# Performance work log

Hardware: AMD Instinct MI355X
Metric: run time of the kernel (lower is better)

Reference implementation:

```python
import jax, jax.numpy as jnp
import numpy as np
import math

U = 1024      # units
H = 16        # num_head
DH = U // H   # units_head
B = 2
Q = 1024      # query length
M = 1024      # memory length
KL = M + Q    # key length
R = KL + 1    # relative positions length (rel-shift needs k_len+1)
EPS = 1e-7    # K.epsilon()


def setup_inputs() -> dict:
    key = jax.random.key(0)
    ks = jax.random.split(key, 11)
    f32 = jnp.float32
    return {
        "inputs": jax.random.normal(ks[0], (B, Q, U), f32),
        "content": jax.random.normal(ks[1], (B, Q, U), f32),
        "memories": jax.random.normal(ks[2], (B, M, U), f32),
        "relatives": jax.random.normal(ks[3], (B, R, U), f32),
        "segment_mat": jax.random.uniform(ks[4], (B, Q, KL, 2), f32),
        "segment_embed": jax.random.normal(ks[5], (2, U), f32) * 0.02,
        "bias_context": jax.random.normal(ks[6], (U,), f32) * 0.02,
        "bias_relative": jax.random.normal(ks[7], (U,), f32) * 0.02,
        "bias_segment": jax.random.normal(ks[8], (U,), f32) * 0.02,
        "permutation": jax.random.uniform(ks[9], (B, Q, KL), f32),
        "kernel": jax.random.normal(ks[10], (U, 5 * U), f32) * 0.02,
    }


def _heads(x):
    # [B, L, U] -> [B, H, L, DH]
    b, l, _ = x.shape
    return x.reshape(b, l, H, DH).transpose(0, 2, 1, 3)


def _rel_shift(x, klen):
    # Transformer-XL relative shift via reshape trick. x: [B, H, Q, R]
    b, h, q, r = x.shape
    x = x.reshape(b, h, r, q)[:, :, 1:, :].reshape(b, h, q, r - 1)
    return x[:, :, :, :klen]


def reference(inputs, content, memories, relatives, segment_mat, segment_embed,
              bias_context, bias_relative, bias_segment, permutation, kernel):
    k_q = kernel[:, :U]
    k_kv = kernel[:, U:3 * U]
    k_r = kernel[:, 3 * U:4 * U]
    k_o = kernel[:, 4 * U:5 * U]

    full = jnp.concatenate([memories, content], axis=1)          # [B, KL, U]
    w_q = inputs @ k_q                                           # [B, Q, U]
    w_kv = full @ k_kv                                           # [B, KL, 2U]
    w_r = relatives @ k_r                                        # [B, R, U]

    w_k = _heads(w_kv[..., :U])                                  # [B, H, KL, DH]
    w_v = _heads(w_kv[..., U:])                                  # [B, H, KL, DH]

    # content term
    q_c = _heads(w_q + bias_context)                             # [B, H, Q, DH]
    a_context = jnp.einsum('bhqd,bhkd->bhqk', q_c, w_k)

    # relative-position term with rel-shift
    q_r = _heads(w_q + bias_relative)
    w_r_h = _heads(w_r)                                          # [B, H, R, DH]
    a_relative = _rel_shift(jnp.einsum('bhqd,bhrd->bhqr', q_r, w_r_h), KL)

    # segment term
    q_s = _heads(w_q + bias_segment)                             # [B, H, Q, DH]
    seg_e = segment_embed.T.reshape(H, DH, 2)                    # [H, DH, 2]
    qs_seg = jnp.einsum('bhqd,hds->bhqs', q_s, seg_e)            # [B, H, Q, 2]
    a_segment = jnp.einsum('bqks,bhqs->bhqk', segment_mat, qs_seg)

    att = (a_context + a_relative + a_segment) / math.sqrt(DH)   # [B, H, Q, KL]
    e = jnp.exp(att - jnp.max(att, axis=-1, keepdims=True))
    e = e * permutation[:, None, :, :]
    att = e / (jnp.sum(e, axis=-1, keepdims=True) + EPS)

    out = jnp.einsum('bhqk,bhkd->bhqd', att, w_v)                # [B, H, Q, DH]
    out = out.transpose(0, 2, 1, 3).reshape(inputs.shape[0], Q, U)
    return out @ k_o                                             # [B, Q, U]
```

## Files before the change

### kernel.cpp

```cpp
#include <hip/hip_runtime.h>

typedef __bf16 bf16;
typedef unsigned short u16;
typedef unsigned int u32;
typedef __attribute__((ext_vector_type(8))) __bf16 bf16x8;
typedef __attribute__((ext_vector_type(4))) __bf16 bf16x4;
typedef __attribute__((ext_vector_type(4))) float f32x4;
typedef __attribute__((ext_vector_type(8))) float f32x8;

#define SWZ(r, s) (((r) << 3) + ((s) ^ ((r) & 7)))
#define GSW(r, s) (((r) << 2) + ((s) ^ (((r) >> 1) & 3)))

__device__ __forceinline__ f32x4 mfma16(bf16x8 a, bf16x8 b, f32x4 c) {
  return __builtin_amdgcn_mfma_f32_16x16x32_bf16(a, b, c, 0, 0, 0);
}
__device__ __forceinline__ void gld16(const void* g, void* l) {
  __builtin_amdgcn_global_load_lds((const __attribute__((address_space(1))) void*)g,
                                   (__attribute__((address_space(3))) void*)l, 16, 0, 0);
}

__global__ __launch_bounds__(256) void prep_all(
    const float* __restrict__ inputs, const float* __restrict__ mem,
    const float* __restrict__ cont, const float* __restrict__ rel,
    const float* __restrict__ K, bf16* __restrict__ in_b,
    bf16* __restrict__ full_b, bf16* __restrict__ rel_b, bf16* __restrict__ KT) {
  __shared__ float t[64][68];
  const int bid = blockIdx.x, tid = threadIdx.x;
  if (bid < 1024) {
    size_t i = ((size_t)bid * 256 + tid) * 8;
    f32x8 v = *reinterpret_cast<const f32x8*>(inputs + i);
    *reinterpret_cast<bf16x8*>(in_b + i) = __builtin_convertvector(v, bf16x8);
  } else if (bid < 3072) {
    size_t i = ((size_t)(bid - 1024) * 256 + tid) * 8;
    int row = (int)(i >> 10), col = (int)(i & 1023);
    int b = row >> 11, r = row & 2047;
    const float* src = (r < 1024)
        ? (mem  + (((size_t)(b << 10) + r)          << 10) + col)
        : (cont + (((size_t)(b << 10) + (r - 1024)) << 10) + col);
    f32x8 v = *reinterpret_cast<const f32x8*>(src);
    *reinterpret_cast<bf16x8*>(full_b + i) = __builtin_convertvector(v, bf16x8);
  } else if (bid < 5121) {
    size_t i = ((size_t)(bid - 3072) * 256 + tid) * 8;
    f32x8 v = *reinterpret_cast<const f32x8*>(rel + i);
    *reinterpret_cast<bf16x8*>(rel_b + i) = __builtin_convertvector(v, bf16x8);
  } else {
    const int r = bid - 5121;
    const int n0 = (r % 80) << 6, k0 = (r / 80) << 6;
    for (int idx = tid; idx < 1024; idx += 256) {
      int rr = idx >> 4, c4 = (idx & 15) << 2;
      f32x4 v = *reinterpret_cast<const f32x4*>(K + (size_t)(k0 + rr) * 5120 + n0 + c4);
      t[rr][c4] = v.x; t[rr][c4 + 1] = v.y; t[rr][c4 + 2] = v.z; t[rr][c4 + 3] = v.w;
    }
    __syncthreads();
    for (int idx = tid; idx < 1024; idx += 256) {
      int rr = idx >> 4, c4 = (idx & 15) << 2;
      bf16x4 o = { (bf16)t[c4][rr], (bf16)t[c4 + 1][rr], (bf16)t[c4 + 2][rr], (bf16)t[c4 + 3][rr] };
      *reinterpret_cast<bf16x4*>(KT + (size_t)(n0 + rr) * 1024 + k0 + c4) = o;
    }
  }
}

template<int MT, int OUT_MODE, int KLEN, bool KWRAP>
__device__ __forceinline__ void gemm_body(
    const bf16* __restrict__ A, const bf16* __restrict__ BT,
    void* __restrict__ C0v, void* __restrict__ C1v,
    int m0, int n0, int Mrows, int splitN, bf16* As, bf16* Bs, int tid) {
  const int l = tid & 63, w = tid >> 6;
  const int wn = (w & 1) << 6;
  const int wm = (w >> 1) * (MT / 2);
  constexpr int MFR = MT / 32;
  const int lc = l & 15, l16 = l >> 4;
  f32x4 acc[MFR][4] = {};
  const int r0 = tid >> 2;
  const int sq = tid & 3;
  const int g0 = (sq ^ ((r0 >> 1) & 3)) << 3;

  for (int k0 = 0; k0 < KLEN; k0 += 32) {
    const int kk = KWRAP ? (k0 & 1023) : k0;
    __syncthreads();
    gld16(A  + (size_t)(m0 + r0) * KLEN + k0 + g0, &As[tid << 3]);
    gld16(BT + (size_t)(n0 + r0) * 1024 + kk + g0, &Bs[tid << 3]);
    if (MT == 128)
      gld16(A + (size_t)(m0 + r0 + 64) * KLEN + k0 + g0, &As[(tid + 256) << 3]);
    gld16(BT + (size_t)(n0 + r0 + 64) * 1024 + kk + g0, &Bs[(tid + 256) << 3]);
    __syncthreads();
    bf16x8 af[MFR], bfv[4];
#pragma unroll
    for (int m = 0; m < MFR; ++m)
      af[m] = *reinterpret_cast<const bf16x8*>(&As[GSW(wm + (m << 4) + lc, l16) << 3]);
#pragma unroll
    for (int n = 0; n < 4; ++n)
      bfv[n] = *reinterpret_cast<const bf16x8*>(&Bs[GSW(wn + (n << 4) + lc, l16) << 3]);
#pragma unroll
    for (int m = 0; m < MFR; ++m)
#pragma unroll
      for (int n = 0; n < 4; ++n)
        acc[m][n] = mfma16(af[m], bfv[n], acc[m][n]);
  }
#pragma unroll
  for (int m = 0; m < MFR; ++m) {
    const int rbase = m0 + wm + (m << 4) + (l16 << 2);
#pragma unroll
    for (int n = 0; n < 4; ++n) {
      const int col = n0 + wn + (n << 4) + lc;
      const int cc = (col < splitN) ? col : (col - splitN);
      void* Cv = (col < splitN) ? C0v : C1v;
#pragma unroll
      for (int r = 0; r < 4; ++r) {
        const int row = rbase + r;
        if (row < Mrows) {
          const float v = acc[m][n][r];
          const size_t off = ((size_t)row << 10) + cc;
          if (OUT_MODE == 1) ((bf16*)Cv)[off] = (bf16)v;
          else               ((float*)Cv)[off] = v;
        }
      }
    }
  }
}

__global__ __launch_bounds__(256) void proj_fused(
    const bf16* __restrict__ in_b, const bf16* __restrict__ full_b,
    const bf16* __restrict__ rel_b, const bf16* __restrict__ kT,
    bf16* __restrict__ w_q, bf16* __restrict__ w_k, bf16* __restrict__ w_v,
    bf16* __restrict__ w_rh) {
  __shared__ bf16 As[4096];
  __shared__ bf16 Bs[4096];
  const int bid = blockIdx.x, tid = threadIdx.x;
  if (bid < 256) {
    gemm_body<64, 1, 1024, false>(in_b, kT, w_q, w_q,
                                  (bid >> 3) << 6, (bid & 7) << 7, 2048, 1 << 30, As, Bs, tid);
  } else if (bid < 768) {
    const int r = bid - 256;
    gemm_body<128, 1, 1024, false>(full_b, kT + (1 << 20), w_k, w_v,
                                   (r >> 4) << 7, (r & 15) << 7, 4096, 1024, As, Bs, tid);
  } else {
    const int r = bid - 768;
    gemm_body<64, 1, 1024, false>(rel_b, kT + 3 * (1 << 20), w_rh, w_rh,
                                  (r >> 3) << 6, (r & 7) << 7, 4098, 1 << 30, As, Bs, tid);
  }
}

__global__ __launch_bounds__(256) void out_proj(
    const bf16* __restrict__ a_cat, const bf16* __restrict__ kTo,
    float* __restrict__ out) {
  __shared__ bf16 As[4096];
  __shared__ bf16 Bs[4096];
  const int bid = blockIdx.x, tid = threadIdx.x;
  gemm_body<64, 0, 2048, true>(a_cat, kTo, out, out,
                               (bid >> 3) << 6, (bid & 7) << 7, 2048, 1 << 30, As, Bs, tid);
}

__global__ __launch_bounds__(256) void mid_prep(
    const float* __restrict__ seg_mat, bf16* __restrict__ seg_b,
    const bf16* __restrict__ w_q, const float* __restrict__ bias_s,
    const float* __restrict__ seg_embed, float* __restrict__ qs) {
  const int bid = blockIdx.x, tid = threadIdx.x;
  if (bid < 4096) {
    size_t i = ((size_t)bid * 256 + tid) * 8;
    f32x8 v = *reinterpret_cast<const f32x8*>(seg_mat + i);
    *reinterpret_cast<bf16x8*>(seg_b + i) = __builtin_convertvector(v, bf16x8);
  } else {
    int idx = (bid - 4096) * 256 + tid;
    int q = idx & 1023, h = (idx >> 10) & 15, b = idx >> 14;
    const bf16* wp = w_q + (((size_t)(b << 10) + q) << 10) + (h << 6);
    const float* bp = bias_s + (h << 6);
    const float* e0 = seg_embed + (h << 6);
    const float* e1 = seg_embed + 1024 + (h << 6);
    float s0 = 0.f, s1 = 0.f;
#pragma unroll 8
    for (int d = 0; d < 64; ++d) {
      float v = (float)wp[d] + bp[d];
      s0 = fmaf(v, e0[d], s0);
      s1 = fmaf(v, e1[d], s1);
    }
    qs[((size_t)idx << 1) + 0] = s0;
    qs[((size_t)idx << 1) + 1] = s1;
  }
}

__global__ __launch_bounds__(256) void attn_mfma(
    const bf16* __restrict__ w_q, const bf16* __restrict__ w_k,
    const bf16* __restrict__ w_v, const bf16* __restrict__ w_rh,
    const float* __restrict__ qs_seg, const bf16* __restrict__ seg_b,
    const float* __restrict__ perm, const float* __restrict__ bias_c,
    const float* __restrict__ bias_r, bf16* __restrict__ a_cat) {
  const int id = blockIdx.x;
  const int h  = (id >> 3) & 15;
  const int cg = (id & 7) | ((id >> 7) << 3);
  const int qt = cg & 15, b = cg >> 4;
  const int qi0 = qt << 6;
  const int tid = threadIdx.x;
  const int w = tid >> 6, l = tid & 63;
  const int lc = l & 15, l16 = l >> 4;
  const int w16 = w << 4;
  const int myq = w16 + lc;

  __shared__ bf16 kt[2][2048];
  __shared__ u16  vt[2][2560];
  __shared__ bf16 wbc[8192];
  __shared__ bf16 wb2v[4096];
  __shared__ float artf[3840];
  float* artw = &artf[w * 960];
  u16*   plw  = (u16*)artw;

  auto stageK = [&](int buf, int kj) {
    int r = tid >> 3, s = tid & 7;
    gld16(w_k + ((size_t)((b << 11) + kj + r) << 10) + (h << 6) + ((s ^ (r & 7)) << 3),
          &kt[buf][tid << 3]);
  };
  auto stageWB = [&](int L0, int nrows, int OFF) {
    for (int base = 0; base < nrows; base += 32) {
      int r = (tid >> 3) + base, s = tid & 7;
      int L = L0 + r;
      int slot = (L + OFF) & 127;
      int grow = L > 2048 ? 2048 : L;
      gld16(w_rh + ((size_t)(b * 2049 + grow) << 10) + (h << 6) + ((s ^ (slot & 7)) << 3),
            &wbc[((slot << 3) | s) << 3]);
    }
  };
  auto stageWB2 = [&]() {
    for (int base = 0; base < 64; base += 32) {
      int r = (tid >> 3) + base, s = tid & 7;
      gld16(w_rh + ((size_t)(b * 2049 + r) << 10) + (h << 6) + ((s ^ (r & 7)) << 3),
            &wb2v[((r << 3) | s) << 3]);
    }
  };
  const int kv2 = (tid & 15) << 1, d4 = ((tid >> 4) & 15) << 2, kw = tid & 15;
  auto loadV = [&](int kj, uint2& ra, uint2& rb) {
    const u16* vp = (const u16*)w_v + ((size_t)((b << 11) + kj + kv2) << 10) + (h << 6) + d4;
    ra = *reinterpret_cast<const uint2*>(vp);
    rb = *reinterpret_cast<const uint2*>(vp + 1024);
  };
  auto writeV = [&](int buf, uint2 ra, uint2 rb) {
    u32* vt32 = reinterpret_cast<u32*>(&vt[buf][0]);
    vt32[(d4 + 0) * 20 + kw] = (ra.x & 0xffffu) | (rb.x << 16);
    vt32[(d4 + 1) * 20 + kw] = (ra.x >> 16) | (rb.x & 0xffff0000u);
    vt32[(d4 + 2) * 20 + kw] = (ra.y & 0xffffu) | (rb.y << 16);
    vt32[(d4 + 3) * 20 + kw] = (ra.y >> 16) | (rb.y & 0xffff0000u);
  };
  const size_t qrowg = (size_t)((b << 10) + qi0 + myq);
  auto loadSP = [&](int kj, bf16x8& sA, bf16x8& sB, f32x4& pA, f32x4& pB) {
    const bf16* sp = seg_b + (qrowg * 2048 + kj + (l16 << 2)) * 2;
    sA = *reinterpret_cast<const bf16x8*>(sp);
    sB = *reinterpret_cast<const bf16x8*>(sp + 32);
    const float* pp = perm + qrowg * 2048 + kj + (l16 << 2);
    pA = *reinterpret_cast<const f32x4*>(pp);
    pB = *reinterpret_cast<const f32x4*>(pp + 16);
  };
  auto artWr = [&](int bandcol, f32x4 a_) {
    *reinterpret_cast<f32x4*>(&artw[bandcol * 20 + (l16 << 2)]) = a_;
  };
  auto artRd = [&](int col) -> float {
    return artw[col * 20 + lc];
  };

  stageK(0, 0);
  stageWB(961 - qi0, 96, 7);
  uint2 ra0, rb0;
  loadV(0, ra0, rb0);
  bf16x8 segA_c, segB_c, segA_n = {}, segB_n = {};
  f32x4 pmA_c, pmB_c, pmA_n = {}, pmB_n = {};
  loadSP(0, segA_c, segB_c, pmA_c, pmB_c);

  const float SCLF = 0.125f * 1.44269504f;
  const int dlo = l16 << 3;
  bf16x8 qcf0, qcf1, qrf0, qrf1, qrg0, qrg1;
  {
    const bf16* qb  = w_q + ((qrowg) << 10) + (h << 6);
    const int rq1 = (qi0 + myq + 1 > 1023) ? 1023 : qi0 + myq + 1;
    const bf16* qb1 = w_q + (((size_t)(b << 10) + rq1) << 10) + (h << 6);
    f32x8 bc0 = *reinterpret_cast<const f32x8*>(bias_c + (h << 6) + dlo);
    f32x8 bc1 = *reinterpret_cast<const f32x8*>(bias_c + (h << 6) + 32 + dlo);
    f32x8 br0 = *reinterpret_cast<const f32x8*>(bias_r + (h << 6) + dlo);
    f32x8 br1 = *reinterpret_cast<const f32x8*>(bias_r + (h << 6) + 32 + dlo);
    bf16x8 q0 = *reinterpret_cast<const bf16x8*>(qb + dlo);
    bf16x8 q1 = *reinterpret_cast<const bf16x8*>(qb + 32 + dlo);
    bf16x8 p0 = *reinterpret_cast<const bf16x8*>(qb1 + dlo);
    bf16x8 p1 = *reinterpret_cast<const bf16x8*>(qb1 + 32 + dlo);
    qcf0 = __builtin_convertvector((__builtin_convertvector(q0, f32x8) + bc0) * SCLF, bf16x8);
    qcf1 = __builtin_convertvector((__builtin_convertvector(q1, f32x8) + bc1) * SCLF, bf16x8);
    qrf0 = __builtin_convertvector((__builtin_convertvector(q0, f32x8) + br0) * SCLF, bf16x8);
    qrf1 = __builtin_convertvector((__builtin_convertvector(q1, f32x8) + br1) * SCLF, bf16x8);
    qrg0 = __builtin_convertvector((__builtin_convertvector(p0, f32x8) + br0) * SCLF, bf16x8);
    qrg1 = __builtin_convertvector((__builtin_convertvector(p1, f32x8) + br1) * SCLF, bf16x8);
  }
  const float* qp = qs_seg + ((((size_t)((b << 4) + h) << 10) + qi0 + myq) << 1);
  const float qs0 = qp[0] * SCLF, qs1 = qp[1] * SCLF;

  writeV(0, ra0, rb0);
  __syncthreads();

  float mrow = -1e30f, lrow = 0.f;
  f32x4 o[4] = {};
  int cur = 0;
  uint2 ra_n = {}, rb_n = {};

  for (int t = 0; t < 64; ++t) {
    const int kj = t << 5;
    const int rel0 = kj - qi0;
    const bool strad = (rel0 == 1024) | (rel0 == 1056);
    const bool mainB = (rel0 >= 1088);
    const bool spec1088 = (rel0 == 1088);
    const int nxt = cur ^ 1;

    if (t < 63) {
      const int kjn = kj + 32, rel0n = rel0 + 32;
      stageK(nxt, kjn);
      if (rel0n == 1024) stageWB2();
      if (rel0n <= 1056)       stageWB(rel0n + 1025, 32, 7);
      else if (rel0n == 1088)  stageWB(64, 32, 8);
      else if (rel0n == 1120) { stageWB(32, 32, 8); stageWB(96, 32, 8); }
      else                     stageWB(rel0n - 1024, 32, 8);
      loadV(kjn, ra_n, rb_n);
      loadSP(kjn, segA_n, segB_n, pmA_n, pmB_n);
    }

    f32x4 s0 = {0.f, 0.f, 0.f, 0.f}, s1 = {0.f, 0.f, 0.f, 0.f};
    {
      const bf16* ktc = kt[cur];
      bf16x8 a0 = *reinterpret_cast<const bf16x8*>(&ktc[SWZ(lc, l16) << 3]);
      bf16x8 a1 = *reinterpret_cast<const bf16x8*>(&ktc[SWZ(lc, l16 + 4) << 3]);
      bf16x8 a2 = *reinterpret_cast<const bf16x8*>(&ktc[SWZ(16 + lc, l16) << 3]);
      bf16x8 a3 = *reinterpret_cast<const bf16x8*>(&ktc[SWZ(16 + lc, l16 + 4) << 3]);
      s0 = mfma16(a0, qcf0, s0); s0 = mfma16(a1, qcf1, s0);
      s1 = mfma16(a2, qcf0, s1); s1 = mfma16(a3, qcf1, s1);
    }

    float relv[8];
    {
      const bf16x8 ar0 = mainB ? qrg0 : qrf0;
      const bf16x8 ar1 = mainB ? qrg1 : qrf1;
      int sbase;
      if (!mainB) sbase = (rel0 + 1016 - w16) & 127;
      else        sbase = (rel0 - 1032 - w16) & 127;
#pragma unroll
      for (int bg = 0; bg < 3; ++bg) {
        bf16x8 w0, w1;
        if (spec1088) {
          int Lr = 48 - w16 + (bg << 4) + lc;
          const bf16* p0 = (Lr < 64) ? &wb2v[SWZ(Lr, l16) << 3]
                                     : &wbc[SWZ((Lr + 8) & 127, l16) << 3];
          const bf16* p1 = (Lr < 64) ? &wb2v[SWZ(Lr, l16 + 4) << 3]
                                     : &wbc[SWZ((Lr + 8) & 127, l16 + 4) << 3];
          w0 = *reinterpret_cast<const bf16x8*>(p0);
          w1 = *reinterpret_cast<const bf16x8*>(p1);
        } else {
          int prow = (sbase + (bg << 4) + lc) & 127;
          w0 = *reinterpret_cast<const bf16x8*>(&wbc[SWZ(prow, l16) << 3]);
          w1 = *reinterpret_cast<const bf16x8*>(&wbc[SWZ(prow, l16 + 4) << 3]);
        }
        f32x4 a_ = {0.f, 0.f, 0.f, 0.f};
        a_ = mfma16(ar0, w0, a_); a_ = mfma16(ar1, w1, a_);
        artWr((bg << 4) + lc, a_);
      }
#pragma unroll
      for (int jj = 0; jj < 4; ++jj) {
        relv[jj]     = artRd(15 + (l16 << 2) + jj - lc);
        relv[4 + jj] = artRd(31 + (l16 << 2) + jj - lc);
      }
      if (strad) {
#pragma unroll
        for (int bg = 0; bg < 3; ++bg) {
          int srow = rel0 - 1040 - w16 + (bg << 4) + lc;
          srow = srow < 0 ? 0 : (srow > 63 ? 63 : srow);
          bf16x8 w0 = *reinterpret_cast<const bf16x8*>(&wb2v[SWZ(srow, l16) << 3]);
          bf16x8 w1 = *reinterpret_cast<const bf16x8*>(&wb2v[SWZ(srow, l16 + 4) << 3]);
          f32x4 a_ = {0.f, 0.f, 0.f, 0.f};
          a_ = mfma16(qrg0, w0, a_); a_ = mfma16(qrg1, w1, a_);
          artWr((bg << 4) + lc, a_);
        }
#pragma unroll
        for (int jj = 0; jj < 4; ++jj) {
          const int jA = (l16 << 2) + jj, jB = 16 + jA;
          float rbA = artRd(15 + jA - lc);
          float rbB = artRd(15 + jB - lc);
          if (rel0 + jA - myq >= 1025) relv[jj] = rbA;
          if (rel0 + jB - myq >= 1025) relv[4 + jj] = rbB;
        }
      }
    }

    bool full;
    float facr;
    {
      f32x8 sgA = __builtin_convertvector(segA_c, f32x8);
      f32x8 sgB = __builtin_convertvector(segB_c, f32x8);
      float sv[8];
#pragma unroll
      for (int jj = 0; jj < 4; ++jj) {
        sv[jj]     = s0[jj] + relv[jj]     + sgA[2 * jj] * qs0 + sgA[2 * jj + 1] * qs1;
        sv[4 + jj] = s1[jj] + relv[4 + jj] + sgB[2 * jj] * qs0 + sgB[2 * jj + 1] * qs1;
      }
      float tm = sv[0];
#pragma unroll
      for (int jj = 1; jj < 8; ++jj) tm = fmaxf(tm, sv[jj]);
      tm = fmaxf(tm, __shfl_xor(tm, 16));
      tm = fmaxf(tm, __shfl_xor(tm, 32));
      full = __any(tm > mrow + 8.f);
      if (full) {
        const float mn2 = fmaxf(mrow, tm);
        facr = exp2f(mrow - mn2);
        mrow = mn2;
      } else {
        facr = 1.f;
      }
      float e[8], rs = 0.f;
#pragma unroll
      for (int jj = 0; jj < 4; ++jj) {
        e[jj]     = exp2f(sv[jj] - mrow) * pmA_c[jj];
        e[4 + jj] = exp2f(sv[4 + jj] - mrow) * pmB_c[jj];
        rs += e[jj] + e[4 + jj];
      }
      rs += __shfl_xor(rs, 16);
      rs += __shfl_xor(rs, 32);
      lrow = lrow * facr + rs;
      bf16x4 pa, pb;
#pragma unroll
      for (int jj = 0; jj < 4; ++jj) { pa[jj] = (bf16)e[jj]; pb[jj] = (bf16)e[4 + jj]; }
      *reinterpret_cast<bf16x4*>(&plw[lc * 40 + (l16 << 2)]) = pa;
      *reinterpret_cast<bf16x4*>(&plw[lc * 40 + 16 + (l16 << 2)]) = pb;
    }

    {
      if (full) {
        const int r4 = l16 << 2;
        float fr0 = __shfl(facr, r4 + 0);
        float fr1 = __shfl(facr, r4 + 1);
        float fr2 = __shfl(facr, r4 + 2);
        float fr3 = __shfl(facr, r4 + 3);
#pragma unroll
        for (int n = 0; n < 4; ++n) {
          o[n][0] *= fr0; o[n][1] *= fr1; o[n][2] *= fr2; o[n][3] *= fr3;
        }
      }
      bf16x8 ap = *reinterpret_cast<const bf16x8*>(&plw[lc * 40 + (l16 << 3)]);
      bf16x8 bv0 = *reinterpret_cast<const bf16x8*>(&vt[cur][(lc) * 40 + (l16 << 3)]);
      bf16x8 bv1 = *reinterpret_cast<const bf16x8*>(&vt[cur][(16 + lc) * 40 + (l16 << 3)]);
      bf16x8 bv2 = *reinterpret_cast<const bf16x8*>(&vt[cur][(32 + lc) * 40 + (l16 << 3)]);
      bf16x8 bv3 = *reinterpret_cast<const bf16x8*>(&vt[cur][(48 + lc) * 40 + (l16 << 3)]);
      o[0] = mfma16(ap, bv0, o[0]);
      o[1] = mfma16(ap, bv1, o[1]);
      o[2] = mfma16(ap, bv2, o[2]);
      o[3] = mfma16(ap, bv3, o[3]);
    }

    if (t < 63) {
      writeV(nxt, ra_n, rb_n);
      segA_c = segA_n; segB_c = segB_n; pmA_c = pmA_n; pmB_c = pmB_n;
    }
    __syncthreads();
    cur = nxt;
  }

  {
    float inv[4];
#pragma unroll
    for (int r = 0; r < 4; ++r)
      inv[r] = 1.f / (__shfl(lrow, (l16 << 2) + r) + 1e-7f);
#pragma unroll
    for (int n = 0; n < 4; ++n) {
#pragma unroll
      for (int r = 0; r < 4; ++r) {
        const int row = qi0 + w16 + (l16 << 2) + r;
        const float v = o[n][r] * inv[r];
        const bf16 hi = (bf16)v;
        const float lof = v - (float)hi;
        const size_t off = (((size_t)(b << 10) + row) << 11) + (h << 6) + (n << 4) + lc;
        a_cat[off] = hi;
        a_cat[off + 1024] = (bf16)lof;
      }
    }
  }
}

extern "C" void kernel_launch(void* const* d_in, const int* in_sizes, int n_in,
                              void* d_out, int out_size, void* d_ws, size_t ws_size,
                              hipStream_t stream) {
  (void)in_sizes; (void)n_in; (void)out_size; (void)ws_size;
  const float* inputs    = (const float*)d_in[0];
  const float* content   = (const float*)d_in[1];
  const float* memories  = (const float*)d_in[2];
  const float* relatives = (const float*)d_in[3];
  const float* seg_mat   = (const float*)d_in[4];
  const float* seg_embed = (const float*)d_in[5];
  const float* bias_c    = (const float*)d_in[6];
  const float* bias_r    = (const float*)d_in[7];
  const float* bias_s    = (const float*)d_in[8];
  const float* perm      = (const float*)d_in[9];
  const float* kern      = (const float*)d_in[10];
  float* out = (float*)d_out;

  char* ws = (char*)d_ws;
  bf16*  in_b   = (bf16*)(ws);
  bf16*  full_b = (bf16*)(ws + 4194304);
  bf16*  rel_b  = (bf16*)(ws + 12582912);
  bf16*  kT     = (bf16*)(ws + 21233664);
  bf16*  w_q    = (bf16*)(ws + 31719424);
  bf16*  w_k    = (bf16*)(ws + 35913728);
  bf16*  w_v    = (bf16*)(ws + 44302336);
  bf16*  w_rh   = (bf16*)(ws + 52690944);
  float* qs     = (float*)(ws + 65277952);
  bf16*  seg_b  = (bf16*)(ws);
  bf16*  a_cat  = (bf16*)(ws + 21233664);
  bf16*  kTo    = (bf16*)(ws + 29622272);

  dim3 blk(256);
  prep_all<<<6401, blk, 0, stream>>>(inputs, memories, content, relatives, kern,
                                     in_b, full_b, rel_b, kT);
  proj_fused<<<1288, blk, 0, stream>>>(in_b, full_b, rel_b, kT, w_q, w_k, w_v, w_rh);
  mid_prep<<<4224, blk, 0, stream>>>(seg_mat, seg_b, w_q, bias_s, seg_embed, qs);
  attn_mfma<<<512, blk, 0, stream>>>(w_q, w_k, w_v, w_rh, qs, seg_b, perm,
                                     bias_c, bias_r, a_cat);
  out_proj<<<256, blk, 0, stream>>>(a_cat, kTo, out);
}
```

Measured before the change: 260.6 us.

## Fuse segment-matrix conversion and segment query projection into attention kernel

```diff
diff --git a/kernel.cpp b/kernel.cpp
--- a/kernel.cpp
+++ b/kernel.cpp
@@ -151,40 +151,13 @@
                                (bid >> 3) << 6, (bid & 7) << 7, 2048, 1 << 30, As, Bs, tid);
 }
 
-__global__ __launch_bounds__(256) void mid_prep(
-    const float* __restrict__ seg_mat, bf16* __restrict__ seg_b,
-    const bf16* __restrict__ w_q, const float* __restrict__ bias_s,
-    const float* __restrict__ seg_embed, float* __restrict__ qs) {
-  const int bid = blockIdx.x, tid = threadIdx.x;
-  if (bid < 4096) {
-    size_t i = ((size_t)bid * 256 + tid) * 8;
-    f32x8 v = *reinterpret_cast<const f32x8*>(seg_mat + i);
-    *reinterpret_cast<bf16x8*>(seg_b + i) = __builtin_convertvector(v, bf16x8);
-  } else {
-    int idx = (bid - 4096) * 256 + tid;
-    int q = idx & 1023, h = (idx >> 10) & 15, b = idx >> 14;
-    const bf16* wp = w_q + (((size_t)(b << 10) + q) << 10) + (h << 6);
-    const float* bp = bias_s + (h << 6);
-    const float* e0 = seg_embed + (h << 6);
-    const float* e1 = seg_embed + 1024 + (h << 6);
-    float s0 = 0.f, s1 = 0.f;
-#pragma unroll 8
-    for (int d = 0; d < 64; ++d) {
-      float v = (float)wp[d] + bp[d];
-      s0 = fmaf(v, e0[d], s0);
-      s1 = fmaf(v, e1[d], s1);
-    }
-    qs[((size_t)idx << 1) + 0] = s0;
-    qs[((size_t)idx << 1) + 1] = s1;
-  }
-}
-
 __global__ __launch_bounds__(256) void attn_mfma(
     const bf16* __restrict__ w_q, const bf16* __restrict__ w_k,
     const bf16* __restrict__ w_v, const bf16* __restrict__ w_rh,
-    const float* __restrict__ qs_seg, const bf16* __restrict__ seg_b,
-    const float* __restrict__ perm, const float* __restrict__ bias_c,
-    const float* __restrict__ bias_r, bf16* __restrict__ a_cat) {
+    const float* __restrict__ seg_mat, const float* __restrict__ perm,
+    const float* __restrict__ bias_c, const float* __restrict__ bias_r,
+    const float* __restrict__ bias_s, const float* __restrict__ seg_embed,
+    bf16* __restrict__ a_cat) {
   const int id = blockIdx.x;
   const int h  = (id >> 3) & 15;
   const int cg = (id & 7) | ((id >> 7) << 3);
@@ -201,6 +174,7 @@
   __shared__ bf16 wbc[8192];
   __shared__ bf16 wb2v[4096];
   __shared__ float artf[3840];
+  __shared__ float facw[64], lroww[64];
   float* artw = &artf[w * 960];
   u16*   plw  = (u16*)artw;
 
@@ -240,10 +214,10 @@
     vt32[(d4 + 3) * 20 + kw] = (ra.y >> 16) | (rb.y & 0xffff0000u);
   };
   const size_t qrowg = (size_t)((b << 10) + qi0 + myq);
-  auto loadSP = [&](int kj, bf16x8& sA, bf16x8& sB, f32x4& pA, f32x4& pB) {
-    const bf16* sp = seg_b + (qrowg * 2048 + kj + (l16 << 2)) * 2;
-    sA = *reinterpret_cast<const bf16x8*>(sp);
-    sB = *reinterpret_cast<const bf16x8*>(sp + 32);
+  auto loadSP = [&](int kj, f32x8& sA, f32x8& sB, f32x4& pA, f32x4& pB) {
+    const float* sp = seg_mat + (qrowg * 2048 + kj + (l16 << 2)) * 2;
+    sA = *reinterpret_cast<const f32x8*>(sp);
+    sB = *reinterpret_cast<const f32x8*>(sp + 32);
     const float* pp = perm + qrowg * 2048 + kj + (l16 << 2);
     pA = *reinterpret_cast<const f32x4*>(pp);
     pB = *reinterpret_cast<const f32x4*>(pp + 16);
@@ -259,13 +233,14 @@
   stageWB(961 - qi0, 96, 7);
   uint2 ra0, rb0;
   loadV(0, ra0, rb0);
-  bf16x8 segA_c, segB_c, segA_n = {}, segB_n = {};
+  f32x8 segA_c, segB_c, segA_n = {}, segB_n = {};
   f32x4 pmA_c, pmB_c, pmA_n = {}, pmB_n = {};
   loadSP(0, segA_c, segB_c, pmA_c, pmB_c);
 
   const float SCLF = 0.125f * 1.44269504f;
   const int dlo = l16 << 3;
   bf16x8 qcf0, qcf1, qrf0, qrf1, qrg0, qrg1;
+  float qs0, qs1;
   {
     const bf16* qb  = w_q + ((qrowg) << 10) + (h << 6);
     const int rq1 = (qi0 + myq + 1 > 1023) ? 1023 : qi0 + myq + 1;
@@ -278,15 +253,31 @@
     bf16x8 q1 = *reinterpret_cast<const bf16x8*>(qb + 32 + dlo);
     bf16x8 p0 = *reinterpret_cast<const bf16x8*>(qb1 + dlo);
     bf16x8 p1 = *reinterpret_cast<const bf16x8*>(qb1 + 32 + dlo);
-    qcf0 = __builtin_convertvector((__builtin_convertvector(q0, f32x8) + bc0) * SCLF, bf16x8);
-    qcf1 = __builtin_convertvector((__builtin_convertvector(q1, f32x8) + bc1) * SCLF, bf16x8);
-    qrf0 = __builtin_convertvector((__builtin_convertvector(q0, f32x8) + br0) * SCLF, bf16x8);
-    qrf1 = __builtin_convertvector((__builtin_convertvector(q1, f32x8) + br1) * SCLF, bf16x8);
+    f32x8 qf0 = __builtin_convertvector(q0, f32x8);
+    f32x8 qf1 = __builtin_convertvector(q1, f32x8);
+    qcf0 = __builtin_convertvector((qf0 + bc0) * SCLF, bf16x8);
+    qcf1 = __builtin_convertvector((qf1 + bc1) * SCLF, bf16x8);
+    qrf0 = __builtin_convertvector((qf0 + br0) * SCLF, bf16x8);
+    qrf1 = __builtin_convertvector((qf1 + br1) * SCLF, bf16x8);
     qrg0 = __builtin_convertvector((__builtin_convertvector(p0, f32x8) + br0) * SCLF, bf16x8);
     qrg1 = __builtin_convertvector((__builtin_convertvector(p1, f32x8) + br1) * SCLF, bf16x8);
-  }
-  const float* qp = qs_seg + ((((size_t)((b << 4) + h) << 10) + qi0 + myq) << 1);
-  const float qs0 = qp[0] * SCLF, qs1 = qp[1] * SCLF;
+    f32x8 bs0 = *reinterpret_cast<const f32x8*>(bias_s + (h << 6) + dlo);
+    f32x8 bs1 = *reinterpret_cast<const f32x8*>(bias_s + (h << 6) + 32 + dlo);
+    f32x8 e00 = *reinterpret_cast<const f32x8*>(seg_embed + (h << 6) + dlo);
+    f32x8 e01 = *reinterpret_cast<const f32x8*>(seg_embed + (h << 6) + 32 + dlo);
+    f32x8 e10 = *reinterpret_cast<const f32x8*>(seg_embed + 1024 + (h << 6) + dlo);
+    f32x8 e11 = *reinterpret_cast<const f32x8*>(seg_embed + 1024 + (h << 6) + 32 + dlo);
+    f32x8 qa = qf0 + bs0, qb2 = qf1 + bs1;
+    float t0 = 0.f, t1 = 0.f;
+#pragma unroll
+    for (int j = 0; j < 8; ++j) {
+      t0 = fmaf(qa[j], e00[j], fmaf(qb2[j], e01[j], t0));
+      t1 = fmaf(qa[j], e10[j], fmaf(qb2[j], e11[j], t1));
+    }
+    t0 += __shfl_xor(t0, 16); t0 += __shfl_xor(t0, 32);
+    t1 += __shfl_xor(t1, 16); t1 += __shfl_xor(t1, 32);
+    qs0 = t0 * SCLF; qs1 = t1 * SCLF;
+  }
 
   writeV(0, ra0, rb0);
   __syncthreads();
@@ -381,35 +372,26 @@
       }
     }
 
-    bool full;
-    float facr;
     {
-      f32x8 sgA = __builtin_convertvector(segA_c, f32x8);
-      f32x8 sgB = __builtin_convertvector(segB_c, f32x8);
       float sv[8];
 #pragma unroll
       for (int jj = 0; jj < 4; ++jj) {
-        sv[jj]     = s0[jj] + relv[jj]     + sgA[2 * jj] * qs0 + sgA[2 * jj + 1] * qs1;
-        sv[4 + jj] = s1[jj] + relv[4 + jj] + sgB[2 * jj] * qs0 + sgB[2 * jj + 1] * qs1;
+        sv[jj]     = s0[jj] + relv[jj]     + segA_c[2 * jj] * qs0 + segA_c[2 * jj + 1] * qs1;
+        sv[4 + jj] = s1[jj] + relv[4 + jj] + segB_c[2 * jj] * qs0 + segB_c[2 * jj + 1] * qs1;
       }
       float tm = sv[0];
 #pragma unroll
       for (int jj = 1; jj < 8; ++jj) tm = fmaxf(tm, sv[jj]);
       tm = fmaxf(tm, __shfl_xor(tm, 16));
       tm = fmaxf(tm, __shfl_xor(tm, 32));
-      full = __any(tm > mrow + 8.f);
-      if (full) {
-        const float mn2 = fmaxf(mrow, tm);
-        facr = exp2f(mrow - mn2);
-        mrow = mn2;
-      } else {
-        facr = 1.f;
-      }
+      const float mn2 = fmaxf(mrow, tm);
+      const float facr = exp2f(mrow - mn2);
+      mrow = mn2;
       float e[8], rs = 0.f;
 #pragma unroll
       for (int jj = 0; jj < 4; ++jj) {
-        e[jj]     = exp2f(sv[jj] - mrow) * pmA_c[jj];
-        e[4 + jj] = exp2f(sv[4 + jj] - mrow) * pmB_c[jj];
+        e[jj]     = exp2f(sv[jj] - mn2) * pmA_c[jj];
+        e[4 + jj] = exp2f(sv[4 + jj] - mn2) * pmB_c[jj];
         rs += e[jj] + e[4 + jj];
       }
       rs += __shfl_xor(rs, 16);
@@ -420,19 +402,16 @@
       for (int jj = 0; jj < 4; ++jj) { pa[jj] = (bf16)e[jj]; pb[jj] = (bf16)e[4 + jj]; }
       *reinterpret_cast<bf16x4*>(&plw[lc * 40 + (l16 << 2)]) = pa;
       *reinterpret_cast<bf16x4*>(&plw[lc * 40 + 16 + (l16 << 2)]) = pb;
+      if (l16 == 0) facw[myq] = facr;
     }
 
     {
-      if (full) {
-        const int r4 = l16 << 2;
-        float fr0 = __shfl(facr, r4 + 0);
-        float fr1 = __shfl(facr, r4 + 1);
-        float fr2 = __shfl(facr, r4 + 2);
-        float fr3 = __shfl(facr, r4 + 3);
-#pragma unroll
-        for (int n = 0; n < 4; ++n) {
-          o[n][0] *= fr0; o[n][1] *= fr1; o[n][2] *= fr2; o[n][3] *= fr3;
-        }
+      float fr[4];
+#pragma unroll
+      for (int r = 0; r < 4; ++r) fr[r] = facw[w16 + (l16 << 2) + r];
+#pragma unroll
+      for (int n = 0; n < 4; ++n) {
+        o[n][0] *= fr[0]; o[n][1] *= fr[1]; o[n][2] *= fr[2]; o[n][3] *= fr[3];
       }
       bf16x8 ap = *reinterpret_cast<const bf16x8*>(&plw[lc * 40 + (l16 << 3)]);
       bf16x8 bv0 = *reinterpret_cast<const bf16x8*>(&vt[cur][(lc) * 40 + (l16 << 3)]);
@@ -453,11 +432,12 @@
     cur = nxt;
   }
 
+  if (l16 == 0) lroww[myq] = lrow;
   {
     float inv[4];
 #pragma unroll
     for (int r = 0; r < 4; ++r)
-      inv[r] = 1.f / (__shfl(lrow, (l16 << 2) + r) + 1e-7f);
+      inv[r] = 1.f / (lroww[w16 + (l16 << 2) + r] + 1e-7f);
 #pragma unroll
     for (int n = 0; n < 4; ++n) {
 #pragma unroll
@@ -500,8 +480,6 @@
   bf16*  w_k    = (bf16*)(ws + 35913728);
   bf16*  w_v    = (bf16*)(ws + 44302336);
   bf16*  w_rh   = (bf16*)(ws + 52690944);
-  float* qs     = (float*)(ws + 65277952);
-  bf16*  seg_b  = (bf16*)(ws);
   bf16*  a_cat  = (bf16*)(ws + 21233664);
   bf16*  kTo    = (bf16*)(ws + 29622272);
 
@@ -509,8 +487,7 @@
   prep_all<<<6401, blk, 0, stream>>>(inputs, memories, content, relatives, kern,
                                      in_b, full_b, rel_b, kT);
   proj_fused<<<1288, blk, 0, stream>>>(in_b, full_b, rel_b, kT, w_q, w_k, w_v, w_rh);
-  mid_prep<<<4224, blk, 0, stream>>>(seg_mat, seg_b, w_q, bias_s, seg_embed, qs);
-  attn_mfma<<<512, blk, 0, stream>>>(w_q, w_k, w_v, w_rh, qs, seg_b, perm,
-                                     bias_c, bias_r, a_cat);
+  attn_mfma<<<512, blk, 0, stream>>>(w_q, w_k, w_v, w_rh, seg_mat, perm,
+                                     bias_c, bias_r, bias_s, seg_embed, a_cat);
   out_proj<<<256, blk, 0, stream>>>(a_cat, kTo, out);
 }
```

Result: slower. 267.3 us (+2.6%).
